# Performance work log

Hardware: AMD Instinct MI355X
Metric: run time of the kernel (lower is better)

The kernel has to match this reference:

```python
import jax, jax.numpy as jnp
import numpy as np

B, S, H = 32, 64, 512
ATT = 128


def _window_index_tables(seq_len):
    # Enumerate all contiguous windows of size 2..S, same set (order-independent
    # for the softmax-weighted sum) as the torch double loop.
    starts, ends = [], []
    for w in range(2, seq_len + 1):
        for s in range(0, seq_len - w + 1):
            starts.append(s)
            ends.append(s + w)
    starts = np.asarray(starts, np.int32)
    ends = np.asarray(ends, np.int32)
    widths = ends - starts
    ks = np.floor(np.log2(widths)).astype(np.int32)  # sparse-table level per window
    e2 = ends - (1 << ks)                            # second gather position
    return starts, e2, ks


def setup_inputs() -> dict:
    key = jax.random.key(0)
    k0, k1, k2, k3, k4 = jax.random.split(key, 5)
    return {
        "lstm_out": jax.random.normal(k0, (B, S, H), dtype=jnp.float32),
        "W1": jax.random.normal(k1, (H, ATT), dtype=jnp.float32) * 0.05,
        "b1": jax.random.normal(k2, (ATT,), dtype=jnp.float32) * 0.05,
        "W2": jax.random.normal(k3, (ATT, 1), dtype=jnp.float32) * 0.05,
        "b2": jax.random.normal(k4, (1,), dtype=jnp.float32) * 0.05,
    }


def reference(lstm_out, W1, b1, W2, b2):
    b, s, h = lstm_out.shape
    # Sparse table: M[k][:, i] = max over lstm_out[:, i : i+2^k] (clipped to s).
    n_levels = int(np.floor(np.log2(s))) + 1
    tables = [lstm_out]
    for k in range(1, n_levels):
        half = 1 << (k - 1)
        prev = tables[-1]
        shifted = jnp.concatenate(
            [prev[:, half:], jnp.full((b, half, h), -jnp.inf, prev.dtype)], axis=1)
        tables.append(jnp.maximum(prev, shifted))
    Mstack = jnp.stack(tables)  # [K, B, S, H]

    starts, e2, ks = _window_index_tables(s)
    # Range max of each window = max of two overlapping power-of-two blocks.
    pooled = jnp.maximum(Mstack[ks, :, starts], Mstack[ks, :, e2])  # [n_win, B, H]
    pooled = jnp.transpose(pooled, (1, 0, 2))  # [B, n_win, H]

    hid = jax.nn.relu(jnp.einsum("bnh,ha->bna", pooled, W1) + b1)
    scores = jnp.einsum("bna,ao->bno", hid, W2) + b2  # [B, n_win, 1]
    attn = jax.nn.softmax(scores, axis=1)
    return jnp.sum(attn * pooled, axis=1)  # [B, H]
```

## Files before the change

kernel.cpp:

```cpp
#include <hip/hip_runtime.h>
#include <stdint.h>


typedef unsigned short u16;
typedef unsigned int u32;

#define B_    32
#define S_    64
#define H_    512
#define ATT_  128
#define NWIN  2016
#define NLEV  7
#define TLEV  6

typedef __bf16 bf16x8 __attribute__((ext_vector_type(8)));
typedef float  f32x4  __attribute__((ext_vector_type(4)));

__device__ __forceinline__ float asf(u32 i) {
  union { u32 i; float f; } v; v.i = i; return v.f;
}
__device__ __forceinline__ u32 asu(float f) {
  union { float f; u32 i; } v; v.f = f; return v.i;
}
__device__ __forceinline__ float bf2f(u16 u) { return asf(((u32)u) << 16); }
__device__ __forceinline__ u16 f2bf(float f) {
  u32 i = asu(f);
  i += 0x7fffu + ((i >> 16) & 1u);
  return (u16)(i >> 16);
}
__device__ __forceinline__ u32 bfmax2(u32 a, u32 b) {
  float a0 = asf(a << 16), a1 = asf(a & 0xffff0000u);
  float b0 = asf(b << 16), b1 = asf(b & 0xffff0000u);
  u32 m0 = asu(fmaxf(a0, b0)), m1 = asu(fmaxf(a1, b1));
  return (m1 & 0xffff0000u) | (m0 >> 16);
}
__device__ __forceinline__ uint4 bfmax8(uint4 a, uint4 b) {
  uint4 m;
  m.x = bfmax2(a.x, b.x); m.y = bfmax2(a.y, b.y);
  m.z = bfmax2(a.z, b.z); m.w = bfmax2(a.w, b.w);
  return m;
}
__device__ __forceinline__ bf16x8 as_bf16x8(uint4 v) {
  union { uint4 u; bf16x8 h; } c; c.u = v; return c.h;
}

__launch_bounds__(256)
__global__ void k01_init(const float* __restrict__ lstm, const float* __restrict__ W1,
                         u16* __restrict__ table, u16* __restrict__ w1tf,
                         u16* __restrict__ widx) {
  int bid = blockIdx.x, tid = threadIdx.x;
  __shared__ u16 bufA[64 * 64], bufB[64 * 64];
  if (bid < 256) {
    int hc = bid & 7, b = bid >> 3;
    const float* src = lstm + (size_t)b * S_ * H_ + hc * 64;
    u16* tb = table + (size_t)b * TLEV * S_ * H_ + hc * 64;
    for (int t = tid; t < 64 * 16; t += 256) {
      int r = t >> 4, c4 = t & 15;
      float4 f = *reinterpret_cast<const float4*>(src + r * H_ + c4 * 4);
      ushort4 u;
      u.x = f2bf(f.x); u.y = f2bf(f.y); u.z = f2bf(f.z); u.w = f2bf(f.w);
      *reinterpret_cast<ushort4*>(&bufA[r * 64 + c4 * 4]) = u;
    }
    u16* pa = bufA; u16* pb = bufB;
    for (int k = 1; k < NLEV; ++k) {
      __syncthreads();
      int half = 1 << (k - 1);
      u16* dst_g = tb + (size_t)(k - 1) * S_ * H_;
      for (int t = tid; t < 64 * 16; t += 256) {
        int r = t >> 4, c4 = t & 15;
        int r2 = r + half; if (r2 > 63) r2 = 63;
        uint2 a  = *reinterpret_cast<const uint2*>(&pa[r  * 64 + c4 * 4]);
        uint2 bq = *reinterpret_cast<const uint2*>(&pa[r2 * 64 + c4 * 4]);
        uint2 m; m.x = bfmax2(a.x, bq.x); m.y = bfmax2(a.y, bq.y);
        *reinterpret_cast<uint2*>(&pb[r * 64 + c4 * 4]) = m;
        *reinterpret_cast<uint2*>(dst_g + r * H_ + c4 * 4) = m;
      }
      u16* tmp = pa; pa = pb; pb = tmp;
    }
  } else {
    int gb = bid - 256;
    if (gb == 0) {
      for (int n = tid; n < NWIN; n += 256) {
        int w = 2, rem = n;
        while (rem >= 65 - w) { rem -= 65 - w; ++w; }
        int s = rem;
        int k = 31 - __clz(w);
        int e2 = s + w - (1 << k);
        widx[n] = (u16)(s | (e2 << 6) | (k << 12));
      }
    }
    for (int q = tid; q < 2048; q += 256) {
      int idx = gb * 2048 + q;
      int e = idx & 7, L = (idx >> 3) & 63, j = (idx >> 9) & 7;
      int k2i = (idx >> 12) & 1, kc = idx >> 13;
      int n  = j * 16 + (L & 15);
      int kq = kc * 64 + k2i * 32 + (L >> 4) * 8 + e;
      w1tf[idx] = f2bf(W1[kq * ATT_ + n]);
    }
  }
}

__launch_bounds__(256)
__attribute__((amdgpu_waves_per_eu(1, 4)))
__global__ void k2_scores(const u16* __restrict__ table, const u16* __restrict__ w1tf,
                          const float* __restrict__ b1, const float* __restrict__ w2,
                          const u16* __restrict__ widx, float* __restrict__ scores) {
  const int b = blockIdx.y, mt = blockIdx.x;
  __shared__ u16 Ts[128 * 64];
  __shared__ u16 widx_l[64];
  __shared__ float b1s[128], w2s[128];
  int tid = threadIdx.x;
  if (tid < 64) {
    int n = mt * 64 + tid; if (n > NWIN - 1) n = NWIN - 1;
    widx_l[tid] = widx[n];
  }
  if (tid < 128) { b1s[tid] = b1[tid]; w2s[tid] = w2[tid]; }
  __syncthreads();

  const int lv_lo = widx_l[0] >> 12;
  const u16* tb = table + (size_t)b * TLEV * S_ * H_ + (size_t)(lv_lo - 1) * S_ * H_;

  int t0 = tid, t1 = tid + 256, t2 = tid + 512, t3 = tid + 768;
  int r0 = t0 >> 3, r1 = t1 >> 3, r2 = t2 >> 3, r3 = t3 >> 3;
  int c0 = t0 & 7,  c1 = t1 & 7,  c2 = t2 & 7,  c3 = t3 & 7;
  const u16* ts0 = tb + r0 * H_ + c0 * 8;
  const u16* ts1 = tb + r1 * H_ + c1 * 8;
  const u16* ts2 = tb + r2 * H_ + c2 * 8;
  const u16* ts3 = tb + r3 * H_ + c3 * 8;
  int sd0 = r0 * 64 + ((c0 ^ (r0 & 7)) * 8);
  int sd1 = r1 * 64 + ((c1 ^ (r1 & 7)) * 8);
  int sd2 = r2 * 64 + ((c2 ^ (r2 & 7)) * 8);
  int sd3 = r3 * 64 + ((c3 ^ (r3 & 7)) * 8);

  int wid = tid >> 6, lane = tid & 63;
  int lrow = lane & 15, quad = lane >> 4;

  int aoff[2][2];
  {
    int pk = widx_l[wid * 16 + lrow];
    int s = pk & 63, e2 = (pk >> 6) & 63, lv = (pk >> 12) - lv_lo;
    int rs = lv * 64 + s, re = lv * 64 + e2;
#pragma unroll
    for (int k2i = 0; k2i < 2; ++k2i) {
      int c = quad + k2i * 4;
      aoff[k2i][0] = rs * 64 + ((c ^ (rs & 7)) * 8);
      aoff[k2i][1] = re * 64 + ((c ^ (re & 7)) * 8);
    }
  }
  const u16* wb = w1tf + lane * 8;

  uint4 rT0, rT1, rT2, rT3;

#define ISSUE(KK) do { \
  rT0 = *reinterpret_cast<const uint4*>(ts0 + (KK)); \
  rT1 = *reinterpret_cast<const uint4*>(ts1 + (KK)); \
  rT2 = *reinterpret_cast<const uint4*>(ts2 + (KK)); \
  rT3 = *reinterpret_cast<const uint4*>(ts3 + (KK)); \
} while (0)

#define STAGE() do { \
  *reinterpret_cast<uint4*>(&Ts[sd0]) = rT0; \
  *reinterpret_cast<uint4*>(&Ts[sd1]) = rT1; \
  *reinterpret_cast<uint4*>(&Ts[sd2]) = rT2; \
  *reinterpret_cast<uint4*>(&Ts[sd3]) = rT3; \
} while (0)

  ISSUE(0);

  f32x4 acc[8];
#pragma unroll
  for (int j = 0; j < 8; ++j) acc[j] = (f32x4){0.f, 0.f, 0.f, 0.f};

  for (int kc = 0; kc < 8; ++kc) {
    __syncthreads();
    STAGE();
    __syncthreads();
    if (kc < 7) ISSUE((kc + 1) * 64);
#pragma unroll
    for (int k2i = 0; k2i < 2; ++k2i) {
      uint4 va = *reinterpret_cast<const uint4*>(&Ts[aoff[k2i][0]]);
      uint4 vb = *reinterpret_cast<const uint4*>(&Ts[aoff[k2i][1]]);
      bf16x8 af = as_bf16x8(bfmax8(va, vb));
      const u16* wbk = wb + (kc * 16 + k2i * 8) * 512;
#pragma unroll
      for (int j = 0; j < 8; ++j) {
        bf16x8 bfr = *reinterpret_cast<const bf16x8*>(wbk + j * 512);
        acc[j] = __builtin_amdgcn_mfma_f32_16x16x32_bf16(af, bfr, acc[j], 0, 0, 0);
      }
    }
  }

#undef ISSUE
#undef STAGE

#pragma unroll
  for (int r = 0; r < 4; ++r) {
    float p = 0.f;
#pragma unroll
    for (int j = 0; j < 8; ++j) {
      int n = j * 16 + lrow;
      float v = acc[j][r] + b1s[n];
      p += (v > 0.f ? v : 0.f) * w2s[n];
    }
    p += __shfl_xor(p, 1, 16);
    p += __shfl_xor(p, 2, 16);
    p += __shfl_xor(p, 4, 16);
    p += __shfl_xor(p, 8, 16);
    if (lrow == 0) {
      int nw = mt * 64 + wid * 16 + quad * 4 + r;
      if (nw < NWIN) scores[b * NWIN + nw] = p;
    }
  }
}

__launch_bounds__(256)
__global__ void k34_out(const u16* __restrict__ table, const float* __restrict__ scores,
                        const u16* __restrict__ widx, float* __restrict__ out) {
  int hc = blockIdx.x, b = blockIdx.y, tid = threadIdx.x;
  __shared__ u16 Tl[6 * 64 * 32];
  __shared__ float attn_l[NWIN];
  __shared__ u16 widx_l[NWIN];
  __shared__ float red[8][32];
  __shared__ float wredM[4], wredS[4];
  const u16* tb = table + (size_t)b * TLEV * S_ * H_;
  int h0 = hc * 32;
  int lane = tid & 63, wid = tid >> 6;

  for (int t = tid; t < 6 * 64 * 4; t += 256) {
    int row = t >> 2, c = t & 3;
    uint4 v = *reinterpret_cast<const uint4*>(tb + row * H_ + h0 + c * 8);
    *reinterpret_cast<uint4*>(&Tl[row * 32 + c * 8]) = v;
  }
  for (int n = tid; n < NWIN; n += 256) widx_l[n] = widx[n];

  float mx = -1e30f;
  for (int n = tid; n < NWIN; n += 256) {
    float v = scores[b * NWIN + n];
    attn_l[n] = v;
    mx = fmaxf(mx, v);
  }
#pragma unroll
  for (int off = 32; off > 0; off >>= 1) mx = fmaxf(mx, __shfl_xor(mx, off, 64));
  if (lane == 0) wredM[wid] = mx;
  __syncthreads();
  mx = fmaxf(fmaxf(wredM[0], wredM[1]), fmaxf(wredM[2], wredM[3]));
  float sum = 0.f;
  for (int n = tid; n < NWIN; n += 256) {
    float e = __expf(attn_l[n] - mx);
    attn_l[n] = e;
    sum += e;
  }
#pragma unroll
  for (int off = 32; off > 0; off >>= 1) sum += __shfl_xor(sum, off, 64);
  if (lane == 0) wredS[wid] = sum;
  __syncthreads();
  float inv = 1.f / (wredS[0] + wredS[1] + wredS[2] + wredS[3]);

  int h = tid & 31, g = tid >> 5;
  float acc = 0.f;
  for (int n = g * 252; n < g * 252 + 252; ++n) {
    int pk = widx_l[n];
    int s = pk & 63, e2 = (pk >> 6) & 63, lv = pk >> 12;
    float va = bf2f(Tl[((lv - 1) * 64 + s) * 32 + h]);
    float vb = bf2f(Tl[((lv - 1) * 64 + e2) * 32 + h]);
    acc += attn_l[n] * fmaxf(va, vb);
  }
  red[g][h] = acc;
  __syncthreads();
  if (tid < 32) {
    float s2 = 0.f;
#pragma unroll
    for (int g2 = 0; g2 < 8; ++g2) s2 += red[g2][tid];
    out[b * H_ + h0 + tid] = s2 * inv;
  }
}

extern "C" void kernel_launch(void* const* d_in, const int* in_sizes, int n_in,
                              void* d_out, int out_size, void* d_ws, size_t ws_size,
                              hipStream_t stream) {
  const float* lstm = (const float*)d_in[0];
  const float* W1   = (const float*)d_in[1];
  const float* b1   = (const float*)d_in[2];
  const float* W2   = (const float*)d_in[3];
  float* out = (float*)d_out;

  char* ws = (char*)d_ws;
  u16*   widx   = (u16*)(ws + 0);
  u16*   w1tf   = (u16*)(ws + 4096);
  u16*   table  = (u16*)(ws + 135168);
  float* scores = (float*)(ws + 12718080);

  k01_init <<<288, 256, 0, stream>>>(lstm, W1, table, w1tf, widx);
  k2_scores<<<dim3(32, B_), 256, 0, stream>>>(table, w1tf, b1, W2, widx, scores);
  k34_out  <<<dim3(16, B_), 256, 0, stream>>>(table, scores, widx, out);
}
```

Before: 138.8 us.

## Stage W1 tiles through LDS in scores kernel and halve output-kernel H chunk

The scores kernel now loads each 8192-element W1 chunk cooperatively into shared memory alongside the table tile, using the same register double-buffered prefetch. The MFMA B operands are then read from LDS instead of straight from global memory. This is meant to cut redundant global/L2 traffic and latency on the weight reads, at the cost of 16KB more LDS per block, which may lower occupancy. Separately, the output kernel handles 16 hidden columns per block instead of 32 and launches twice as many blocks. That doubles parallelism in that stage but also repeats the softmax work per block.

```diff
diff --git a/kernel.cpp b/kernel.cpp
--- a/kernel.cpp
+++ b/kernel.cpp
@@ -107,6 +107,7 @@
                           const u16* __restrict__ widx, float* __restrict__ scores) {
   const int b = blockIdx.y, mt = blockIdx.x;
   __shared__ u16 Ts[128 * 64];
+  __shared__ u16 Bs[8192];
   __shared__ u16 widx_l[64];
   __shared__ float b1s[128], w2s[128];
   int tid = threadIdx.x;
@@ -131,6 +132,7 @@
   int sd1 = r1 * 64 + ((c1 ^ (r1 & 7)) * 8);
   int sd2 = r2 * 64 + ((c2 ^ (r2 & 7)) * 8);
   int sd3 = r3 * 64 + ((c3 ^ (r3 & 7)) * 8);
+  int bo0 = tid * 8, bo1 = bo0 + 2048, bo2 = bo0 + 4096, bo3 = bo0 + 6144;
 
   int wid = tid >> 6, lane = tid & 63;
   int lrow = lane & 15, quad = lane >> 4;
@@ -147,15 +149,20 @@
       aoff[k2i][1] = re * 64 + ((c ^ (re & 7)) * 8);
     }
   }
-  const u16* wb = w1tf + lane * 8;
-
-  uint4 rT0, rT1, rT2, rT3;
-
-#define ISSUE(KK) do { \
-  rT0 = *reinterpret_cast<const uint4*>(ts0 + (KK)); \
-  rT1 = *reinterpret_cast<const uint4*>(ts1 + (KK)); \
-  rT2 = *reinterpret_cast<const uint4*>(ts2 + (KK)); \
-  rT3 = *reinterpret_cast<const uint4*>(ts3 + (KK)); \
+
+  uint4 rT0, rT1, rT2, rT3, rB0, rB1, rB2, rB3;
+
+#define ISSUE(KC) do { \
+  int kk_ = (KC) * 64; \
+  const u16* wsrc_ = w1tf + (KC) * 8192; \
+  rT0 = *reinterpret_cast<const uint4*>(ts0 + kk_); \
+  rT1 = *reinterpret_cast<const uint4*>(ts1 + kk_); \
+  rT2 = *reinterpret_cast<const uint4*>(ts2 + kk_); \
+  rT3 = *reinterpret_cast<const uint4*>(ts3 + kk_); \
+  rB0 = *reinterpret_cast<const uint4*>(wsrc_ + bo0); \
+  rB1 = *reinterpret_cast<const uint4*>(wsrc_ + bo1); \
+  rB2 = *reinterpret_cast<const uint4*>(wsrc_ + bo2); \
+  rB3 = *reinterpret_cast<const uint4*>(wsrc_ + bo3); \
 } while (0)
 
 #define STAGE() do { \
@@ -163,6 +170,10 @@
   *reinterpret_cast<uint4*>(&Ts[sd1]) = rT1; \
   *reinterpret_cast<uint4*>(&Ts[sd2]) = rT2; \
   *reinterpret_cast<uint4*>(&Ts[sd3]) = rT3; \
+  *reinterpret_cast<uint4*>(&Bs[bo0]) = rB0; \
+  *reinterpret_cast<uint4*>(&Bs[bo1]) = rB1; \
+  *reinterpret_cast<uint4*>(&Bs[bo2]) = rB2; \
+  *reinterpret_cast<uint4*>(&Bs[bo3]) = rB3; \
 } while (0)
 
   ISSUE(0);
@@ -175,16 +186,16 @@
     __syncthreads();
     STAGE();
     __syncthreads();
-    if (kc < 7) ISSUE((kc + 1) * 64);
+    if (kc < 7) ISSUE(kc + 1);
 #pragma unroll
     for (int k2i = 0; k2i < 2; ++k2i) {
       uint4 va = *reinterpret_cast<const uint4*>(&Ts[aoff[k2i][0]]);
       uint4 vb = *reinterpret_cast<const uint4*>(&Ts[aoff[k2i][1]]);
       bf16x8 af = as_bf16x8(bfmax8(va, vb));
-      const u16* wbk = wb + (kc * 16 + k2i * 8) * 512;
+      const u16* bk = &Bs[k2i * 4096 + lane * 8];
 #pragma unroll
       for (int j = 0; j < 8; ++j) {
-        bf16x8 bfr = *reinterpret_cast<const bf16x8*>(wbk + j * 512);
+        bf16x8 bfr = *reinterpret_cast<const bf16x8*>(bk + j * 512);
         acc[j] = __builtin_amdgcn_mfma_f32_16x16x32_bf16(af, bfr, acc[j], 0, 0, 0);
       }
     }
@@ -217,19 +228,19 @@
 __global__ void k34_out(const u16* __restrict__ table, const float* __restrict__ scores,
                         const u16* __restrict__ widx, float* __restrict__ out) {
   int hc = blockIdx.x, b = blockIdx.y, tid = threadIdx.x;
-  __shared__ u16 Tl[6 * 64 * 32];
+  __shared__ u16 Tl[6 * 64 * 16];
   __shared__ float attn_l[NWIN];
   __shared__ u16 widx_l[NWIN];
-  __shared__ float red[8][32];
+  __shared__ float red[16][16];
   __shared__ float wredM[4], wredS[4];
   const u16* tb = table + (size_t)b * TLEV * S_ * H_;
-  int h0 = hc * 32;
+  int h0 = hc * 16;
   int lane = tid & 63, wid = tid >> 6;
 
-  for (int t = tid; t < 6 * 64 * 4; t += 256) {
-    int row = t >> 2, c = t & 3;
+  for (int t = tid; t < 6 * 64 * 2; t += 256) {
+    int row = t >> 1, c = t & 1;
     uint4 v = *reinterpret_cast<const uint4*>(tb + row * H_ + h0 + c * 8);
-    *reinterpret_cast<uint4*>(&Tl[row * 32 + c * 8]) = v;
+    *reinterpret_cast<uint4*>(&Tl[row * 16 + c * 8]) = v;
   }
   for (int n = tid; n < NWIN; n += 256) widx_l[n] = widx[n];
 
@@ -256,21 +267,21 @@
   __syncthreads();
   float inv = 1.f / (wredS[0] + wredS[1] + wredS[2] + wredS[3]);
 
-  int h = tid & 31, g = tid >> 5;
+  int h = tid & 15, g = tid >> 4;
   float acc = 0.f;
-  for (int n = g * 252; n < g * 252 + 252; ++n) {
+  for (int n = g * 126; n < g * 126 + 126; ++n) {
     int pk = widx_l[n];
     int s = pk & 63, e2 = (pk >> 6) & 63, lv = pk >> 12;
-    float va = bf2f(Tl[((lv - 1) * 64 + s) * 32 + h]);
-    float vb = bf2f(Tl[((lv - 1) * 64 + e2) * 32 + h]);
+    float va = bf2f(Tl[((lv - 1) * 64 + s) * 16 + h]);
+    float vb = bf2f(Tl[((lv - 1) * 64 + e2) * 16 + h]);
     acc += attn_l[n] * fmaxf(va, vb);
   }
   red[g][h] = acc;
   __syncthreads();
-  if (tid < 32) {
+  if (tid < 16) {
     float s2 = 0.f;
 #pragma unroll
-    for (int g2 = 0; g2 < 8; ++g2) s2 += red[g2][tid];
+    for (int g2 = 0; g2 < 16; ++g2) s2 += red[g2][tid];
     out[b * H_ + h0 + tid] = s2 * inv;
   }
 }
@@ -292,5 +303,5 @@
 
   k01_init <<<288, 256, 0, stream>>>(lstm, W1, table, w1tf, widx);
   k2_scores<<<dim3(32, B_), 256, 0, stream>>>(table, w1tf, b1, W2, widx, scores);
-  k34_out  <<<dim3(16, B_), 256, 0, stream>>>(table, scores, widx, out);
-}
+  k34_out  <<<dim3(32, B_), 256, 0, stream>>>(table, scores, widx, out);
+}
```

Measured after the change: 118.1 us. 1.18x faster.
